# Kernel optimization log

Measured on AMD Instinct MI355X. Metric: run time of the kernel, lower is better.

Reference implementation:

```python
import math
import jax, jax.numpy as jnp
import numpy as np

SQRT_2_OVER_PI = 0.7978845608028654
FACIL_RATE = 2.0
FIRE_THRESH = 0.88
EPS = 1e-05

def _gelu(x):
    return 0.5 * x * (1.0 + jnp.tanh(SQRT_2_OVER_PI * (x + 0.044715 * x ** 3)))

def setup_inputs() -> dict:
    key = jax.random.key(0)
    ks = jax.random.split(key, 8)
    B, T, D, N = 4, 4096, 1024, 512
    x = jax.random.normal(ks[0], (B, T, D), jnp.float32)
    ema_x = jax.random.normal(ks[1], (D,), jnp.float32) * 0.1
    ema_x2 = ema_x ** 2 + jax.random.uniform(ks[2], (D,), jnp.float32) + 0.5
    ema_y = jax.random.normal(ks[3], (D,), jnp.float32) * 0.1
    ema_y2 = ema_y ** 2 + jax.random.uniform(ks[4], (D,), jnp.float32) + 0.5
    buf = jax.random.normal(ks[5], (N, D), jnp.float32)
    buf = buf / jnp.linalg.norm(buf, axis=-1, keepdims=True)
    facil = 1.0 + 2.0 * jax.random.uniform(ks[6], (N,), jnp.float32)  # facilitation levels >= 1
    mask = jnp.ones((N,), dtype=bool)
    return {
        'x': x,
        'log_tau_in': jnp.float32(math.log(1.0)),
        'log_tau_out': jnp.float32(math.log(1.0)),
        'log_a_in': jnp.float32(0.0),
        'log_a_out': jnp.float32(0.0),
        'log_k_boost': jnp.float32(math.log(0.5)),
        'log_k_damp': jnp.float32(math.log(0.3)),
        'ema_x': ema_x, 'ema_x2': ema_x2, 'ema_y': ema_y, 'ema_y2': ema_y2,
        'buf': buf, 'facil': facil, 'mask': mask,
    }

def reference(x, log_tau_in, log_tau_out, log_a_in, log_a_out,
              log_k_boost, log_k_damp, ema_x, ema_x2, ema_y, ema_y2,
              buf, facil, mask):
    sg = jax.lax.stop_gradient
    D = x.shape[-1]
    y = _gelu(x)
    # --- gate_211 (l1_ready steady state); z-statistics are detached in torch ---
    tau_in, tau_out = jnp.exp(log_tau_in), jnp.exp(log_tau_out)
    a_in, a_out = jax.nn.sigmoid(log_a_in), jax.nn.sigmoid(log_a_out)
    std_x = jnp.sqrt(jnp.clip(sg(ema_x2) - sg(ema_x) ** 2, 0.0)) + EPS
    z_in = jnp.mean(((sg(x) - sg(ema_x)) / std_x) ** 2, axis=-1)        # [B,T]
    std_y = jnp.sqrt(jnp.clip(sg(ema_y2) - sg(ema_y) ** 2, 0.0)) + EPS
    z_out = jnp.mean(((sg(y) - sg(ema_y)) / std_y) ** 2, axis=-1)       # [B,T]
    g_in = 1.0 - a_in + a_in * jnp.exp(-tau_in * z_in)
    g_out = 1.0 - a_out + a_out * jnp.exp(-tau_out * z_out)
    gate = g_in * g_out
    y1 = y * gate[..., None]
    # --- eval-time OCS nearest-neighbor facilitation (l2_ready, pass1_complete) ---
    k_boost = jnp.clip(jnp.exp(log_k_boost), 0.01, 4.0)
    k_damp = jnp.clip(jnp.exp(log_k_damp), 0.01, 0.9)
    y1_mean = jnp.mean(sg(y1).reshape(-1, D), axis=0)                    # [D]
    m_n = y1_mean / jnp.maximum(jnp.linalg.norm(y1_mean), 1e-12)
    buf_sg = sg(buf)
    buf_n = buf_sg / jnp.maximum(jnp.linalg.norm(buf_sg, axis=-1, keepdims=True), 1e-12)
    sims = jnp.where(mask, buf_n @ m_n, -1.0)                            # [N]
    nearest_idx = jnp.argmax(sims)
    sim_val = jnp.clip(sims[nearest_idx], 0.0, 1.0)
    fired = sim_val > FIRE_THRESH
    facil_level = sg(facil)[nearest_idx] * jnp.where(fired, FACIL_RATE, 1.0)
    v = buf_sg[nearest_idx]                                              # [D]
    valid = jnp.all(jnp.isfinite(v)) & (jnp.linalg.norm(v) >= 1e-06)
    mod = (facil_level - 1.0) * sim_val
    boost = 1.0 + sg(k_boost) * mod            # torch uses .item(): detached
    damp = jnp.maximum(0.01, 1.0 - sg(k_damp) * mod)
    proj = jnp.sum(y1 * v, axis=-1, keepdims=True)
    y_par = proj * v
    out = jnp.where(valid, y_par * boost + (y1 - y_par) * damp, y1)
    return out
```

## Files before the change

kernel.cpp:

```cpp
#include <hip/hip_runtime.h>
#include <math.h>

#define D 1024
#define NROWS 16384
#define NBUF 512

#define OFF_STAT 0
#define OFF_AX   0
#define OFF_BX   1024
#define OFF_AY   2048
#define OFF_BY   3072
#define OFF_MEAN 4096
#define OFF_KEY  5120
#define OFF_CONST 5124
#define OFF_GATE 5632
#define OFF_PART 22016

typedef float nfloat4 __attribute__((ext_vector_type(4)));

__device__ __forceinline__ float4 ld4(const float* p) { return *(const float4*)p; }

__device__ __forceinline__ float wave_red(float v) {
    #pragma unroll
    for (int off = 32; off > 0; off >>= 1) v += __shfl_xor(v, off, 64);
    return v;
}

__device__ __forceinline__ float gelu_f(float x) {
    float x2 = x * x;
    float t1 = fmaf(0.044715f, x2, 1.0f);
    float u2 = (1.5957691216057308f * x) * t1;
    float e  = __expf(u2);
    float r  = __builtin_amdgcn_rcpf(e + 1.0f);
    return fmaf(-x, r, x);
}

__device__ __forceinline__ float4 gelu4(float4 x) {
    float4 y;
    y.x = gelu_f(x.x); y.y = gelu_f(x.y); y.z = gelu_f(x.z); y.w = gelu_f(x.w);
    return y;
}

__global__ void k_init(const float* __restrict__ ema_x, const float* __restrict__ ema_x2,
                       const float* __restrict__ ema_y, const float* __restrict__ ema_y2,
                       const float* __restrict__ lti, const float* __restrict__ lto,
                       const float* __restrict__ lai, const float* __restrict__ lao,
                       float* __restrict__ ws) {
    int t = threadIdx.x;
    if (t < D) {
        float mx = ema_x[t];
        float vx = fmaxf(ema_x2[t] - mx * mx, 0.0f);
        float ax = 1.0f / (sqrtf(vx) + 1e-5f);
        ws[OFF_AX + t] = ax;
        ws[OFF_BX + t] = mx * ax;
        float my = ema_y[t];
        float vy = fmaxf(ema_y2[t] - my * my, 0.0f);
        float ay = 1.0f / (sqrtf(vy) + 1e-5f);
        ws[OFF_AY + t] = ay;
        ws[OFF_BY + t] = my * ay;
        ws[OFF_MEAN + t] = 0.0f;
    }
    if (t == 0) {
        *(unsigned long long*)&ws[OFF_KEY] = 0ull;
        ws[OFF_CONST + 0] = __expf(lti[0]);
        ws[OFF_CONST + 1] = __expf(lto[0]);
        ws[OFF_CONST + 2] = 1.0f / (1.0f + __expf(-lai[0]));
        ws[OFF_CONST + 3] = 1.0f / (1.0f + __expf(-lao[0]));
    }
}

template<int RPW>
__global__ __launch_bounds__(256, 4) void k_passA(const float* __restrict__ x,
                                                  float* __restrict__ ws) {
    __shared__ float s_stat[4096];
    __shared__ float s_acc[D];
    const int tid = threadIdx.x;
    const int wave = tid >> 6, lane = tid & 63;

    for (int i = tid; i < 1024; i += 256) {
        *(float4*)&s_stat[4 * i] = ld4(&ws[OFF_STAT + 4 * i]);
        s_acc[i] = 0.0f;
    }
    __syncthreads();

    const float tau_in = ws[OFF_CONST + 0], tau_out = ws[OFF_CONST + 1];
    const float a_in  = ws[OFF_CONST + 2], a_out  = ws[OFF_CONST + 3];

    int col[4];
    #pragma unroll
    for (int j = 0; j < 4; ++j) col[j] = 4 * lane + 256 * j;

    float4 acc[4];
    #pragma unroll
    for (int j = 0; j < 4; ++j) acc[j] = make_float4(0.f, 0.f, 0.f, 0.f);

    const int r0 = (blockIdx.x * 4 + wave) * RPW;
    for (int r = r0; r < r0 + RPW; ++r) {
        const float* xr = x + (size_t)r * D;
        float4 xv[4];
        #pragma unroll
        for (int j = 0; j < 4; ++j) xv[j] = ld4(&xr[col[j]]);

        float4 yv[4];
        float zin = 0.f, zout = 0.f;
        #pragma unroll
        for (int j = 0; j < 4; ++j) {
            float4 a = *(const float4*)&s_stat[OFF_AX + col[j]];
            float4 b = *(const float4*)&s_stat[OFF_BX + col[j]];
            float dx;
            dx = fmaf(xv[j].x, a.x, -b.x); zin = fmaf(dx, dx, zin);
            dx = fmaf(xv[j].y, a.y, -b.y); zin = fmaf(dx, dx, zin);
            dx = fmaf(xv[j].z, a.z, -b.z); zin = fmaf(dx, dx, zin);
            dx = fmaf(xv[j].w, a.w, -b.w); zin = fmaf(dx, dx, zin);
            yv[j] = gelu4(xv[j]);
            float4 ay = *(const float4*)&s_stat[OFF_AY + col[j]];
            float4 by = *(const float4*)&s_stat[OFF_BY + col[j]];
            float dy;
            dy = fmaf(yv[j].x, ay.x, -by.x); zout = fmaf(dy, dy, zout);
            dy = fmaf(yv[j].y, ay.y, -by.y); zout = fmaf(dy, dy, zout);
            dy = fmaf(yv[j].z, ay.z, -by.z); zout = fmaf(dy, dy, zout);
            dy = fmaf(yv[j].w, ay.w, -by.w); zout = fmaf(dy, dy, zout);
        }
        zin  = wave_red(zin)  * (1.0f / D);
        zout = wave_red(zout) * (1.0f / D);
        float g = ((1.0f - a_in)  + a_in  * __expf(-tau_in  * zin)) *
                  ((1.0f - a_out) + a_out * __expf(-tau_out * zout));
        if (lane == 0) ws[OFF_GATE + r] = g;
        #pragma unroll
        for (int j = 0; j < 4; ++j) {
            acc[j].x = fmaf(yv[j].x, g, acc[j].x);
            acc[j].y = fmaf(yv[j].y, g, acc[j].y);
            acc[j].z = fmaf(yv[j].z, g, acc[j].z);
            acc[j].w = fmaf(yv[j].w, g, acc[j].w);
        }
    }
    #pragma unroll
    for (int j = 0; j < 4; ++j) {
        atomicAdd(&s_acc[col[j] + 0], acc[j].x);
        atomicAdd(&s_acc[col[j] + 1], acc[j].y);
        atomicAdd(&s_acc[col[j] + 2], acc[j].z);
        atomicAdd(&s_acc[col[j] + 3], acc[j].w);
    }
    __syncthreads();
    *(float4*)&ws[OFF_PART + (size_t)blockIdx.x * D + 4 * tid] = *(float4*)&s_acc[4 * tid];
}

__global__ __launch_bounds__(256) void k_mean(float* __restrict__ ws) {
    const int tid = threadIdx.x;
    const float* P = &ws[OFF_PART + (size_t)blockIdx.x * 16 * D];
    float4 s = make_float4(0.f, 0.f, 0.f, 0.f);
    #pragma unroll
    for (int i = 0; i < 16; ++i) {
        float4 v = ld4(&P[(size_t)i * D + 4 * tid]);
        s.x += v.x; s.y += v.y; s.z += v.z; s.w += v.w;
    }
    atomicAdd(&ws[OFF_MEAN + 4 * tid + 0], s.x);
    atomicAdd(&ws[OFF_MEAN + 4 * tid + 1], s.y);
    atomicAdd(&ws[OFF_MEAN + 4 * tid + 2], s.z);
    atomicAdd(&ws[OFF_MEAN + 4 * tid + 3], s.w);
}

__global__ __launch_bounds__(256) void k_sims(const float* __restrict__ buf,
                                              const unsigned char* __restrict__ mask,
                                              float* __restrict__ ws) {
    __shared__ float s_red[4];
    __shared__ float s_inv;
    const int tid = threadIdx.x, wave = tid >> 6, lane = tid & 63;

    float4 mv = ld4(&ws[OFF_MEAN + tid * 4]);
    float ns = mv.x * mv.x + mv.y * mv.y + mv.z * mv.z + mv.w * mv.w;
    ns = wave_red(ns);
    if (lane == 0) s_red[wave] = ns;
    __syncthreads();
    if (tid == 0) {
        float t = s_red[0] + s_red[1] + s_red[2] + s_red[3];
        s_inv = 1.0f / fmaxf(sqrtf(t), 1e-12f);
    }
    __syncthreads();
    const float inv = s_inv;

    int col[4];
    float4 mvv[4];
    #pragma unroll
    for (int j = 0; j < 4; ++j) {
        col[j] = 4 * lane + 256 * j;
        mvv[j] = ld4(&ws[OFF_MEAN + col[j]]);
    }
    const int n = blockIdx.x * 4 + wave;
    const float* br = buf + (size_t)n * D;
    float dot = 0.f, bns = 0.f;
    #pragma unroll
    for (int j = 0; j < 4; ++j) {
        float4 bv = ld4(&br[col[j]]);
        dot += bv.x * mvv[j].x + bv.y * mvv[j].y + bv.z * mvv[j].z + bv.w * mvv[j].w;
        bns += bv.x * bv.x + bv.y * bv.y + bv.z * bv.z + bv.w * bv.w;
    }
    dot = wave_red(dot);
    bns = wave_red(bns);
    if (lane == 0) {
        float sim = -1.0f;
        if (mask[n]) sim = (dot * inv) / fmaxf(sqrtf(bns), 1e-12f);
        unsigned int fb = __float_as_uint(sim);
        unsigned int mono = (fb & 0x80000000u) ? ~fb : (fb | 0x80000000u);
        unsigned long long key = ((unsigned long long)mono << 32) | (unsigned int)(~n);
        atomicMax((unsigned long long*)&ws[OFF_KEY], key);
    }
}

__global__ __launch_bounds__(256, 4) void k_passB(const float* __restrict__ x,
                                                  const float* __restrict__ buf,
                                                  const float* __restrict__ facil,
                                                  const float* __restrict__ lkb,
                                                  const float* __restrict__ lkd,
                                                  const float* __restrict__ ws,
                                                  float* __restrict__ out) {
    __shared__ float s_v[D];
    __shared__ float s_red[4];
    __shared__ float s_sc[3];
    const int tid = threadIdx.x, wave = tid >> 6, lane = tid & 63;

    const unsigned long long key = *(const unsigned long long*)&ws[OFF_KEY];
    const int idx = (int)(~(unsigned int)(key & 0xFFFFFFFFull));
    const unsigned int mono = (unsigned int)(key >> 32);
    const unsigned int fb = (mono & 0x80000000u) ? (mono ^ 0x80000000u) : ~mono;
    const float sim = __uint_as_float(fb);

    float4 vt = ld4(&buf[(size_t)idx * D + 4 * tid]);
    float bns = 0.f;
    if (!isfinite(vt.x) || !isfinite(vt.y) || !isfinite(vt.z) || !isfinite(vt.w))
        bns = __uint_as_float(0x7FC00000u);
    bns += vt.x * vt.x + vt.y * vt.y + vt.z * vt.z + vt.w * vt.w;
    bns = wave_red(bns);
    if (lane == 0) s_red[wave] = bns;
    __syncthreads();
    if (tid == 0) {
        float t = s_red[0] + s_red[1] + s_red[2] + s_red[3];
        int valid = (t >= 1e-12f) ? 1 : 0;
        float sim_val = fminf(fmaxf(sim, 0.0f), 1.0f);
        float fl = facil[idx] * ((sim_val > 0.88f) ? 2.0f : 1.0f);
        float mod = (fl - 1.0f) * sim_val;
        float kb = fminf(fmaxf(__expf(lkb[0]), 0.01f), 4.0f);
        float kd = fminf(fmaxf(__expf(lkd[0]), 0.01f), 0.9f);
        float boost = 1.0f + kb * mod;
        float damp = fmaxf(0.01f, 1.0f - kd * mod);
        s_sc[0] = valid ? damp : 1.0f;
        s_sc[1] = valid ? (boost - damp) : 0.0f;
        s_sc[2] = (float)valid;
    }
    __syncthreads();
    const float dampe = s_sc[0], coef = s_sc[1];
    if (s_sc[2] == 0.0f) vt = make_float4(0.f, 0.f, 0.f, 0.f);
    *(float4*)&s_v[4 * tid] = vt;
    __syncthreads();

    int col[4];
    #pragma unroll
    for (int j = 0; j < 4; ++j) col[j] = 4 * lane + 256 * j;

    const int r0 = (blockIdx.x * 4 + wave) * 2;
    for (int r = r0; r < r0 + 2; ++r) {
        const float* xr = x + (size_t)r * D;
        const float g = ws[OFF_GATE + r];
        float4 y1[4], vv[4];
        float proj = 0.f;
        #pragma unroll
        for (int j = 0; j < 4; ++j) {
            float4 xv = ld4(&xr[col[j]]);
            vv[j] = *(const float4*)&s_v[col[j]];
            y1[j] = gelu4(xv);
            y1[j].x *= g; y1[j].y *= g; y1[j].z *= g; y1[j].w *= g;
            proj = fmaf(y1[j].x, vv[j].x, proj);
            proj = fmaf(y1[j].y, vv[j].y, proj);
            proj = fmaf(y1[j].z, vv[j].z, proj);
            proj = fmaf(y1[j].w, vv[j].w, proj);
        }
        proj = wave_red(proj);
        const float pc = proj * coef;
        float* orow = out + (size_t)r * D;
        #pragma unroll
        for (int j = 0; j < 4; ++j) {
            float4 o;
            o.x = fmaf(y1[j].x, dampe, pc * vv[j].x);
            o.y = fmaf(y1[j].y, dampe, pc * vv[j].y);
            o.z = fmaf(y1[j].z, dampe, pc * vv[j].z);
            o.w = fmaf(y1[j].w, dampe, pc * vv[j].w);
            *(float4*)&orow[col[j]] = o;
        }
    }
}

extern "C" void kernel_launch(void* const* d_in, const int* in_sizes, int n_in,
                              void* d_out, int out_size, void* d_ws, size_t ws_size,
                              hipStream_t stream) {
    const float* x      = (const float*)d_in[0];
    const float* lti    = (const float*)d_in[1];
    const float* lto    = (const float*)d_in[2];
    const float* lai    = (const float*)d_in[3];
    const float* lao    = (const float*)d_in[4];
    const float* lkb    = (const float*)d_in[5];
    const float* lkd    = (const float*)d_in[6];
    const float* ema_x  = (const float*)d_in[7];
    const float* ema_x2 = (const float*)d_in[8];
    const float* ema_y  = (const float*)d_in[9];
    const float* ema_y2 = (const float*)d_in[10];
    const float* buf    = (const float*)d_in[11];
    const float* facil  = (const float*)d_in[12];
    const unsigned char* mask = (const unsigned char*)d_in[13];
    float* ws  = (float*)d_ws;
    float* out = (float*)d_out;

    int NP;
    if      (ws_size >= ((size_t)OFF_PART + 2048u * D) * 4) NP = 2048;
    else if (ws_size >= ((size_t)OFF_PART + 1024u * D) * 4) NP = 1024;
    else                                                    NP = 512;

    hipLaunchKernelGGL(k_init, dim3(1), dim3(1024), 0, stream,
                       ema_x, ema_x2, ema_y, ema_y2, lti, lto, lai, lao, ws);
    if (NP == 2048)
        hipLaunchKernelGGL(k_passA<2>, dim3(2048), dim3(256), 0, stream, x, ws);
    else if (NP == 1024)
        hipLaunchKernelGGL(k_passA<4>, dim3(1024), dim3(256), 0, stream, x, ws);
    else
        hipLaunchKernelGGL(k_passA<8>, dim3(512), dim3(256), 0, stream, x, ws);
    hipLaunchKernelGGL(k_mean, dim3(NP / 16), dim3(256), 0, stream, ws);
    hipLaunchKernelGGL(k_sims, dim3(128), dim3(256), 0, stream, buf, mask, ws);
    hipLaunchKernelGGL(k_passB, dim3(2048), dim3(256), 0, stream,
                       x, buf, facil, lkb, lkd, ws, out);
}
```

Baseline: 214.3 us.

## Fuse all stages into one cooperative persistent kernel with grid syncs

Replaces the five-kernel pipeline (init, passA, mean, sims, passB) with a single cooperative kernel of 1024 blocks that uses grid.sync between the statistics, mean reduction, similarity argmax and output phases. It also stores the per-column normalisation stats as packed fp16 in shared memory, processes two rows at a time, and writes the output with nontemporal stores. The aim is to remove launch gaps and intermediate kernel boundaries. The trade-offs are grid-wide barrier cost, reduced stat precision from fp16, and a fallback to the old path if the cooperative launch fails.

```diff
diff --git a/kernel.cpp b/kernel.cpp
--- a/kernel.cpp
+++ b/kernel.cpp
@@ -1,9 +1,14 @@
 #include <hip/hip_runtime.h>
+#include <hip/hip_cooperative_groups.h>
+#include <hip/hip_fp16.h>
 #include <math.h>
+
+namespace cg = cooperative_groups;
 
 #define D 1024
 #define NROWS 16384
 #define NBUF 512
+#define NBLK 1024
 
 #define OFF_STAT 0
 #define OFF_AX   0
@@ -19,6 +24,10 @@
 typedef float nfloat4 __attribute__((ext_vector_type(4)));
 
 __device__ __forceinline__ float4 ld4(const float* p) { return *(const float4*)p; }
+__device__ __forceinline__ void st4_nt(float* p, float4 v) {
+    nfloat4 nv = { v.x, v.y, v.z, v.w };
+    __builtin_nontemporal_store(nv, (nfloat4*)p);
+}
 
 __device__ __forceinline__ float wave_red(float v) {
     #pragma unroll
@@ -39,6 +48,278 @@
     float4 y;
     y.x = gelu_f(x.x); y.y = gelu_f(x.y); y.z = gelu_f(x.z); y.w = gelu_f(x.w);
     return y;
+}
+
+__device__ __forceinline__ float2 uh2f(unsigned int u) {
+    __half2 h;
+    __builtin_memcpy(&h, &u, 4);
+    return __half22float2(h);
+}
+
+__device__ __forceinline__ unsigned int packh2(float a, float b) {
+    __half2 h = __floats2half2_rn(a, b);
+    unsigned int u;
+    __builtin_memcpy(&u, &h, 4);
+    return u;
+}
+
+__global__ __launch_bounds__(256, 4) void k_fused(
+        const float* __restrict__ x,
+        const float* __restrict__ ema_x,  const float* __restrict__ ema_x2,
+        const float* __restrict__ ema_y,  const float* __restrict__ ema_y2,
+        const float* __restrict__ lti,    const float* __restrict__ lto,
+        const float* __restrict__ lai,    const float* __restrict__ lao,
+        const float* __restrict__ buf,    const float* __restrict__ facil,
+        const float* __restrict__ lkb,    const float* __restrict__ lkd,
+        const unsigned char* __restrict__ mask,
+        float* __restrict__ ws,           float* __restrict__ out) {
+    cg::grid_group grid = cg::this_grid();
+    __shared__ unsigned int s_mem[2048];
+    float* s_f   = (float*)s_mem;
+    float* s_red = (float*)&s_mem[1024];
+    float* s_sc  = (float*)&s_mem[1032];
+    const int tid = threadIdx.x, wave = tid >> 6, lane = tid & 63;
+    const int b = blockIdx.x;
+
+    for (int i = tid; i < 1024; i += 256) {
+        float mx = ema_x[i];
+        float vx = fmaxf(ema_x2[i] - mx * mx, 0.0f);
+        float ax = 1.0f / (sqrtf(vx) + 1e-5f);
+        s_mem[i] = packh2(ax, mx * ax);
+        float my = ema_y[i];
+        float vy = fmaxf(ema_y2[i] - my * my, 0.0f);
+        float ay = 1.0f / (sqrtf(vy) + 1e-5f);
+        s_mem[1024 + i] = packh2(ay, my * ay);
+    }
+    if (b == 0 && tid == 0) *(unsigned long long*)&ws[OFF_KEY] = 0ull;
+    __syncthreads();
+
+    const float tau_in = __expf(lti[0]), tau_out = __expf(lto[0]);
+    const float a_in  = 1.0f / (1.0f + __expf(-lai[0]));
+    const float a_out = 1.0f / (1.0f + __expf(-lao[0]));
+
+    int col[4];
+    #pragma unroll
+    for (int j = 0; j < 4; ++j) col[j] = 4 * lane + 256 * j;
+
+    float4 acc[4];
+    #pragma unroll
+    for (int j = 0; j < 4; ++j) acc[j] = make_float4(0.f, 0.f, 0.f, 0.f);
+
+    const int r0 = (b * 4 + wave) * 4;
+
+    #pragma unroll
+    for (int k = 0; k < 2; ++k) {
+        const int rA = r0 + 2 * k, rB = rA + 1;
+        const float* pA = x + (size_t)rA * D;
+        const float* pB = x + (size_t)rB * D;
+        float4 xA[4], xB[4];
+        #pragma unroll
+        for (int j = 0; j < 4; ++j) { xA[j] = ld4(&pA[col[j]]); xB[j] = ld4(&pB[col[j]]); }
+        float4 yA[4], yB[4];
+        float zinA = 0.f, zoutA = 0.f, zinB = 0.f, zoutB = 0.f;
+        #pragma unroll
+        for (int j = 0; j < 4; ++j) {
+            uint4 ux = *(const uint4*)&s_mem[col[j]];
+            uint4 uy = *(const uint4*)&s_mem[1024 + col[j]];
+            float2 s0 = uh2f(ux.x), s1 = uh2f(ux.y), s2 = uh2f(ux.z), s3 = uh2f(ux.w);
+            float d;
+            d = fmaf(xA[j].x, s0.x, -s0.y); zinA = fmaf(d, d, zinA);
+            d = fmaf(xA[j].y, s1.x, -s1.y); zinA = fmaf(d, d, zinA);
+            d = fmaf(xA[j].z, s2.x, -s2.y); zinA = fmaf(d, d, zinA);
+            d = fmaf(xA[j].w, s3.x, -s3.y); zinA = fmaf(d, d, zinA);
+            d = fmaf(xB[j].x, s0.x, -s0.y); zinB = fmaf(d, d, zinB);
+            d = fmaf(xB[j].y, s1.x, -s1.y); zinB = fmaf(d, d, zinB);
+            d = fmaf(xB[j].z, s2.x, -s2.y); zinB = fmaf(d, d, zinB);
+            d = fmaf(xB[j].w, s3.x, -s3.y); zinB = fmaf(d, d, zinB);
+            yA[j] = gelu4(xA[j]);
+            yB[j] = gelu4(xB[j]);
+            float2 t0 = uh2f(uy.x), t1 = uh2f(uy.y), t2 = uh2f(uy.z), t3 = uh2f(uy.w);
+            d = fmaf(yA[j].x, t0.x, -t0.y); zoutA = fmaf(d, d, zoutA);
+            d = fmaf(yA[j].y, t1.x, -t1.y); zoutA = fmaf(d, d, zoutA);
+            d = fmaf(yA[j].z, t2.x, -t2.y); zoutA = fmaf(d, d, zoutA);
+            d = fmaf(yA[j].w, t3.x, -t3.y); zoutA = fmaf(d, d, zoutA);
+            d = fmaf(yB[j].x, t0.x, -t0.y); zoutB = fmaf(d, d, zoutB);
+            d = fmaf(yB[j].y, t1.x, -t1.y); zoutB = fmaf(d, d, zoutB);
+            d = fmaf(yB[j].z, t2.x, -t2.y); zoutB = fmaf(d, d, zoutB);
+            d = fmaf(yB[j].w, t3.x, -t3.y); zoutB = fmaf(d, d, zoutB);
+        }
+        zinA  = wave_red(zinA)  * (1.0f / D);
+        zinB  = wave_red(zinB)  * (1.0f / D);
+        zoutA = wave_red(zoutA) * (1.0f / D);
+        zoutB = wave_red(zoutB) * (1.0f / D);
+        float gA = ((1.0f - a_in)  + a_in  * __expf(-tau_in  * zinA)) *
+                   ((1.0f - a_out) + a_out * __expf(-tau_out * zoutA));
+        float gB = ((1.0f - a_in)  + a_in  * __expf(-tau_in  * zinB)) *
+                   ((1.0f - a_out) + a_out * __expf(-tau_out * zoutB));
+        if (lane == 0) { ws[OFF_GATE + rA] = gA; ws[OFF_GATE + rB] = gB; }
+        #pragma unroll
+        for (int j = 0; j < 4; ++j) {
+            acc[j].x = fmaf(yA[j].x, gA, fmaf(yB[j].x, gB, acc[j].x));
+            acc[j].y = fmaf(yA[j].y, gA, fmaf(yB[j].y, gB, acc[j].y));
+            acc[j].z = fmaf(yA[j].z, gA, fmaf(yB[j].z, gB, acc[j].z));
+            acc[j].w = fmaf(yA[j].w, gA, fmaf(yB[j].w, gB, acc[j].w));
+        }
+    }
+    __syncthreads();
+    for (int i = tid; i < 1024; i += 256) s_f[i] = 0.0f;
+    __syncthreads();
+    #pragma unroll
+    for (int j = 0; j < 4; ++j) {
+        atomicAdd(&s_f[col[j] + 0], acc[j].x);
+        atomicAdd(&s_f[col[j] + 1], acc[j].y);
+        atomicAdd(&s_f[col[j] + 2], acc[j].z);
+        atomicAdd(&s_f[col[j] + 3], acc[j].w);
+    }
+    __syncthreads();
+    *(float4*)&ws[OFF_PART + (size_t)b * D + 4 * tid] = *(float4*)&s_f[4 * tid];
+
+    grid.sync();
+
+    if (b < 64) {
+        const int g = b * 4 + wave;
+        float4 s = make_float4(0.f, 0.f, 0.f, 0.f);
+        for (int rr = lane; rr < NBLK; rr += 64) {
+            float4 p = ld4(&ws[OFF_PART + (size_t)rr * D + 4 * g]);
+            s.x += p.x; s.y += p.y; s.z += p.z; s.w += p.w;
+        }
+        s.x = wave_red(s.x); s.y = wave_red(s.y);
+        s.z = wave_red(s.z); s.w = wave_red(s.w);
+        if (lane == 0) *(float4*)&ws[OFF_MEAN + 4 * g] = s;
+    }
+
+    grid.sync();
+
+    if (b < 128) {
+        float4 mv = ld4(&ws[OFF_MEAN + 4 * tid]);
+        float ns = mv.x * mv.x + mv.y * mv.y + mv.z * mv.z + mv.w * mv.w;
+        ns = wave_red(ns);
+        if (lane == 0) s_red[wave] = ns;
+        __syncthreads();
+        if (tid == 0) {
+            float t = s_red[0] + s_red[1] + s_red[2] + s_red[3];
+            s_sc[0] = 1.0f / fmaxf(sqrtf(t), 1e-12f);
+        }
+        __syncthreads();
+        const float inv = s_sc[0];
+        float4 mvv[4];
+        #pragma unroll
+        for (int j = 0; j < 4; ++j) mvv[j] = ld4(&ws[OFF_MEAN + col[j]]);
+        const int n = b * 4 + wave;
+        const float* br = buf + (size_t)n * D;
+        float dot = 0.f, bns = 0.f;
+        #pragma unroll
+        for (int j = 0; j < 4; ++j) {
+            float4 bv = ld4(&br[col[j]]);
+            dot = fmaf(bv.x, mvv[j].x, dot); dot = fmaf(bv.y, mvv[j].y, dot);
+            dot = fmaf(bv.z, mvv[j].z, dot); dot = fmaf(bv.w, mvv[j].w, dot);
+            bns = fmaf(bv.x, bv.x, bns); bns = fmaf(bv.y, bv.y, bns);
+            bns = fmaf(bv.z, bv.z, bns); bns = fmaf(bv.w, bv.w, bns);
+        }
+        dot = wave_red(dot);
+        bns = wave_red(bns);
+        if (lane == 0) {
+            float sim = -1.0f;
+            if (mask[n]) sim = (dot * inv) / fmaxf(sqrtf(bns), 1e-12f);
+            unsigned int fb = __float_as_uint(sim);
+            unsigned int mono = (fb & 0x80000000u) ? ~fb : (fb | 0x80000000u);
+            unsigned long long key = ((unsigned long long)mono << 32) | (unsigned int)(~n);
+            atomicMax((unsigned long long*)&ws[OFF_KEY], key);
+        }
+    }
+
+    grid.sync();
+
+    const unsigned long long key = *(volatile unsigned long long*)&ws[OFF_KEY];
+    const int idx = (int)(~(unsigned int)(key & 0xFFFFFFFFull));
+    const unsigned int mono = (unsigned int)(key >> 32);
+    const unsigned int fbv = (mono & 0x80000000u) ? (mono ^ 0x80000000u) : ~mono;
+    const float sim = __uint_as_float(fbv);
+
+    float4 vt = ld4(&buf[(size_t)idx * D + 4 * tid]);
+    float bns2 = 0.f;
+    if (!isfinite(vt.x) || !isfinite(vt.y) || !isfinite(vt.z) || !isfinite(vt.w))
+        bns2 = __uint_as_float(0x7FC00000u);
+    bns2 += vt.x * vt.x + vt.y * vt.y + vt.z * vt.z + vt.w * vt.w;
+    bns2 = wave_red(bns2);
+    if (lane == 0) s_red[wave] = bns2;
+    __syncthreads();
+    if (tid == 0) {
+        float t = s_red[0] + s_red[1] + s_red[2] + s_red[3];
+        int valid = (t >= 1e-12f) ? 1 : 0;
+        float sim_val = fminf(fmaxf(sim, 0.0f), 1.0f);
+        float fl = facil[idx] * ((sim_val > 0.88f) ? 2.0f : 1.0f);
+        float mod = (fl - 1.0f) * sim_val;
+        float kb = fminf(fmaxf(__expf(lkb[0]), 0.01f), 4.0f);
+        float kd = fminf(fmaxf(__expf(lkd[0]), 0.01f), 0.9f);
+        float boost = 1.0f + kb * mod;
+        float damp = fmaxf(0.01f, 1.0f - kd * mod);
+        s_sc[0] = valid ? damp : 1.0f;
+        s_sc[1] = valid ? (boost - damp) : 0.0f;
+        s_sc[2] = (float)valid;
+    }
+    __syncthreads();
+    const float dampe = s_sc[0], coef = s_sc[1];
+    if (s_sc[2] == 0.0f) vt = make_float4(0.f, 0.f, 0.f, 0.f);
+    __syncthreads();
+    *(float4*)&s_f[4 * tid] = vt;
+    __syncthreads();
+
+    float4 vv[4];
+    #pragma unroll
+    for (int j = 0; j < 4; ++j) vv[j] = *(const float4*)&s_f[col[j]];
+
+    #pragma unroll
+    for (int k = 0; k < 2; ++k) {
+        const int rA = r0 + 2 * k, rB = rA + 1;
+        const float gA = ws[OFF_GATE + rA], gB = ws[OFF_GATE + rB];
+        const float* pA = x + (size_t)rA * D;
+        const float* pB = x + (size_t)rB * D;
+        float4 xA[4], xB[4];
+        #pragma unroll
+        for (int j = 0; j < 4; ++j) { xA[j] = ld4(&pA[col[j]]); xB[j] = ld4(&pB[col[j]]); }
+        float4 yA[4], yB[4];
+        float projA = 0.f, projB = 0.f;
+        #pragma unroll
+        for (int j = 0; j < 4; ++j) {
+            yA[j] = gelu4(xA[j]);
+            yA[j].x *= gA; yA[j].y *= gA; yA[j].z *= gA; yA[j].w *= gA;
+            yB[j] = gelu4(xB[j]);
+            yB[j].x *= gB; yB[j].y *= gB; yB[j].z *= gB; yB[j].w *= gB;
+            projA = fmaf(yA[j].x, vv[j].x, projA); projA = fmaf(yA[j].y, vv[j].y, projA);
+            projA = fmaf(yA[j].z, vv[j].z, projA); projA = fmaf(yA[j].w, vv[j].w, projA);
+            projB = fmaf(yB[j].x, vv[j].x, projB); projB = fmaf(yB[j].y, vv[j].y, projB);
+            projB = fmaf(yB[j].z, vv[j].z, projB); projB = fmaf(yB[j].w, vv[j].w, projB);
+        }
+        projA = wave_red(projA);
+        projB = wave_red(projB);
+        const float pcA = projA * coef, pcB = projB * coef;
+        float* oA = out + (size_t)rA * D;
+        float* oB = out + (size_t)rB * D;
+        #pragma unroll
+        for (int j = 0; j < 4; ++j) {
+            float4 o;
+            o.x = fmaf(yA[j].x, dampe, pcA * vv[j].x);
+            o.y = fmaf(yA[j].y, dampe, pcA * vv[j].y);
+            o.z = fmaf(yA[j].z, dampe, pcA * vv[j].z);
+            o.w = fmaf(yA[j].w, dampe, pcA * vv[j].w);
+            st4_nt(&oA[col[j]], o);
+            o.x = fmaf(yB[j].x, dampe, pcB * vv[j].x);
+            o.y = fmaf(yB[j].y, dampe, pcB * vv[j].y);
+            o.z = fmaf(yB[j].z, dampe, pcB * vv[j].z);
+            o.w = fmaf(yB[j].w, dampe, pcB * vv[j].w);
+            st4_nt(&oB[col[j]], o);
+        }
+    }
+}
+
+__device__ __forceinline__ float4 inv_std4(float4 m, float4 m2) {
+    float4 r;
+    r.x = 1.0f / (sqrtf(fmaxf(m2.x - m.x * m.x, 0.f)) + 1e-5f);
+    r.y = 1.0f / (sqrtf(fmaxf(m2.y - m.y * m.y, 0.f)) + 1e-5f);
+    r.z = 1.0f / (sqrtf(fmaxf(m2.z - m.z * m.z, 0.f)) + 1e-5f);
+    r.w = 1.0f / (sqrtf(fmaxf(m2.w - m.w * m.w, 0.f)) + 1e-5f);
+    return r;
 }
 
 __global__ void k_init(const float* __restrict__ ema_x, const float* __restrict__ ema_x2,
@@ -76,31 +357,25 @@
     __shared__ float s_acc[D];
     const int tid = threadIdx.x;
     const int wave = tid >> 6, lane = tid & 63;
-
     for (int i = tid; i < 1024; i += 256) {
         *(float4*)&s_stat[4 * i] = ld4(&ws[OFF_STAT + 4 * i]);
         s_acc[i] = 0.0f;
     }
     __syncthreads();
-
     const float tau_in = ws[OFF_CONST + 0], tau_out = ws[OFF_CONST + 1];
     const float a_in  = ws[OFF_CONST + 2], a_out  = ws[OFF_CONST + 3];
-
     int col[4];
     #pragma unroll
     for (int j = 0; j < 4; ++j) col[j] = 4 * lane + 256 * j;
-
     float4 acc[4];
     #pragma unroll
     for (int j = 0; j < 4; ++j) acc[j] = make_float4(0.f, 0.f, 0.f, 0.f);
-
     const int r0 = (blockIdx.x * 4 + wave) * RPW;
     for (int r = r0; r < r0 + RPW; ++r) {
         const float* xr = x + (size_t)r * D;
         float4 xv[4];
         #pragma unroll
         for (int j = 0; j < 4; ++j) xv[j] = ld4(&xr[col[j]]);
-
         float4 yv[4];
         float zin = 0.f, zout = 0.f;
         #pragma unroll
@@ -166,7 +441,6 @@
     __shared__ float s_red[4];
     __shared__ float s_inv;
     const int tid = threadIdx.x, wave = tid >> 6, lane = tid & 63;
-
     float4 mv = ld4(&ws[OFF_MEAN + tid * 4]);
     float ns = mv.x * mv.x + mv.y * mv.y + mv.z * mv.z + mv.w * mv.w;
     ns = wave_red(ns);
@@ -178,7 +452,6 @@
     }
     __syncthreads();
     const float inv = s_inv;
-
     int col[4];
     float4 mvv[4];
     #pragma unroll
@@ -218,13 +491,11 @@
     __shared__ float s_red[4];
     __shared__ float s_sc[3];
     const int tid = threadIdx.x, wave = tid >> 6, lane = tid & 63;
-
     const unsigned long long key = *(const unsigned long long*)&ws[OFF_KEY];
     const int idx = (int)(~(unsigned int)(key & 0xFFFFFFFFull));
     const unsigned int mono = (unsigned int)(key >> 32);
     const unsigned int fb = (mono & 0x80000000u) ? (mono ^ 0x80000000u) : ~mono;
     const float sim = __uint_as_float(fb);
-
     float4 vt = ld4(&buf[(size_t)idx * D + 4 * tid]);
     float bns = 0.f;
     if (!isfinite(vt.x) || !isfinite(vt.y) || !isfinite(vt.z) || !isfinite(vt.w))
@@ -252,27 +523,25 @@
     if (s_sc[2] == 0.0f) vt = make_float4(0.f, 0.f, 0.f, 0.f);
     *(float4*)&s_v[4 * tid] = vt;
     __syncthreads();
-
     int col[4];
     #pragma unroll
     for (int j = 0; j < 4; ++j) col[j] = 4 * lane + 256 * j;
-
     const int r0 = (blockIdx.x * 4 + wave) * 2;
     for (int r = r0; r < r0 + 2; ++r) {
         const float* xr = x + (size_t)r * D;
         const float g = ws[OFF_GATE + r];
-        float4 y1[4], vv[4];
+        float4 y1[4], vvv[4];
         float proj = 0.f;
         #pragma unroll
         for (int j = 0; j < 4; ++j) {
             float4 xv = ld4(&xr[col[j]]);
-            vv[j] = *(const float4*)&s_v[col[j]];
+            vvv[j] = *(const float4*)&s_v[col[j]];
             y1[j] = gelu4(xv);
             y1[j].x *= g; y1[j].y *= g; y1[j].z *= g; y1[j].w *= g;
-            proj = fmaf(y1[j].x, vv[j].x, proj);
-            proj = fmaf(y1[j].y, vv[j].y, proj);
-            proj = fmaf(y1[j].z, vv[j].z, proj);
-            proj = fmaf(y1[j].w, vv[j].w, proj);
+            proj = fmaf(y1[j].x, vvv[j].x, proj);
+            proj = fmaf(y1[j].y, vvv[j].y, proj);
+            proj = fmaf(y1[j].z, vvv[j].z, proj);
+            proj = fmaf(y1[j].w, vvv[j].w, proj);
         }
         proj = wave_red(proj);
         const float pc = proj * coef;
@@ -280,10 +549,10 @@
         #pragma unroll
         for (int j = 0; j < 4; ++j) {
             float4 o;
-            o.x = fmaf(y1[j].x, dampe, pc * vv[j].x);
-            o.y = fmaf(y1[j].y, dampe, pc * vv[j].y);
-            o.z = fmaf(y1[j].z, dampe, pc * vv[j].z);
-            o.w = fmaf(y1[j].w, dampe, pc * vv[j].w);
+            o.x = fmaf(y1[j].x, dampe, pc * vvv[j].x);
+            o.y = fmaf(y1[j].y, dampe, pc * vvv[j].y);
+            o.z = fmaf(y1[j].z, dampe, pc * vvv[j].z);
+            o.w = fmaf(y1[j].w, dampe, pc * vvv[j].w);
             *(float4*)&orow[col[j]] = o;
         }
     }
@@ -309,21 +578,31 @@
     float* ws  = (float*)d_ws;
     float* out = (float*)d_out;
 
-    int NP;
-    if      (ws_size >= ((size_t)OFF_PART + 2048u * D) * 4) NP = 2048;
-    else if (ws_size >= ((size_t)OFF_PART + 1024u * D) * 4) NP = 1024;
-    else                                                    NP = 512;
-
-    hipLaunchKernelGGL(k_init, dim3(1), dim3(1024), 0, stream,
-                       ema_x, ema_x2, ema_y, ema_y2, lti, lto, lai, lao, ws);
-    if (NP == 2048)
-        hipLaunchKernelGGL(k_passA<2>, dim3(2048), dim3(256), 0, stream, x, ws);
-    else if (NP == 1024)
-        hipLaunchKernelGGL(k_passA<4>, dim3(1024), dim3(256), 0, stream, x, ws);
-    else
-        hipLaunchKernelGGL(k_passA<8>, dim3(512), dim3(256), 0, stream, x, ws);
-    hipLaunchKernelGGL(k_mean, dim3(NP / 16), dim3(256), 0, stream, ws);
-    hipLaunchKernelGGL(k_sims, dim3(128), dim3(256), 0, stream, buf, mask, ws);
-    hipLaunchKernelGGL(k_passB, dim3(2048), dim3(256), 0, stream,
-                       x, buf, facil, lkb, lkd, ws, out);
-}
+    void* args[] = {
+        (void*)&x,
+        (void*)&ema_x, (void*)&ema_x2, (void*)&ema_y, (void*)&ema_y2,
+        (void*)&lti, (void*)&lto, (void*)&lai, (void*)&lao,
+        (void*)&buf, (void*)&facil, (void*)&lkb, (void*)&lkd,
+        (void*)&mask, (void*)&ws, (void*)&out,
+    };
+    hipError_t err = hipLaunchCooperativeKernel((void*)k_fused, dim3(NBLK), dim3(256),
+                                                args, 0, stream);
+    if (err != hipSuccess) {
+        int NP;
+        if      (ws_size >= ((size_t)OFF_PART + 2048u * D) * 4) NP = 2048;
+        else if (ws_size >= ((size_t)OFF_PART + 1024u * D) * 4) NP = 1024;
+        else                                                    NP = 512;
+        hipLaunchKernelGGL(k_init, dim3(1), dim3(1024), 0, stream,
+                           ema_x, ema_x2, ema_y, ema_y2, lti, lto, lai, lao, ws);
+        if (NP == 2048)
+            hipLaunchKernelGGL(k_passA<2>, dim3(2048), dim3(256), 0, stream, x, ws);
+        else if (NP == 1024)
+            hipLaunchKernelGGL(k_passA<4>, dim3(1024), dim3(256), 0, stream, x, ws);
+        else
+            hipLaunchKernelGGL(k_passA<8>, dim3(512), dim3(256), 0, stream, x, ws);
+        hipLaunchKernelGGL(k_mean, dim3(NP / 16), dim3(256), 0, stream, ws);
+        hipLaunchKernelGGL(k_sims, dim3(128), dim3(256), 0, stream, buf, mask, ws);
+        hipLaunchKernelGGL(k_passB, dim3(2048), dim3(256), 0, stream,
+                           x, buf, facil, lkb, lkd, ws, out);
+    }
+}
```

Result: slower. 512.4 us (+139.1%).
